# Kernel tuning notes

Measured on AMD Instinct MI355X. Metric: run time of the kernel, lower is better.

Reference implementation:

```python
import jax, jax.numpy as jnp
import numpy as np

SIZE = 512  # context size
T, D1, D2 = 32768, 512, 512
HID = int(SIZE * 1.5)  # 768, units of the 'context_linear' Dense


def setup_inputs() -> dict:
    key = jax.random.key(0)
    ks = jax.random.split(key, 8)
    din = D1 + D2
    return {
        "x1": jax.random.normal(ks[0], (T, D1), jnp.float32),
        "x2": jax.random.normal(ks[1], (T, D2), jnp.float32),
        "context0": jax.random.normal(ks[2], (1, SIZE), jnp.float32) * 0.1,  # tf.Variable init stddev=0.1
        "W_linear": jax.random.normal(ks[3], (din, HID), jnp.float32) * 0.02,
        "b_linear": jnp.zeros((HID,), jnp.float32),
        "W_embed": jax.random.normal(ks[4], (HID, SIZE), jnp.float32) * 0.02,
        "W_rate": jax.random.normal(ks[5], (SIZE, 1), jnp.float32) * 0.02,
        "W_forget": jax.random.normal(ks[6], (SIZE, SIZE), jnp.float32) * 0.02,
    }


def reference(x1, x2, context0, W_linear, b_linear, W_embed, W_rate, W_forget):
    # z = embed(linear(concat(inputs))) : Dense(1.5*size, linear) -> Dense(size, sigmoid, no bias)
    z = jnp.concatenate([x1, x2], axis=-1)                      # [T, D1+D2]
    z = jax.nn.sigmoid((z @ W_linear + b_linear) @ W_embed)     # [T, SIZE]
    # rate gate depends only on z_t, so precompute it in one GEMM
    r = jnp.tanh(z @ W_rate)[:, 0]                              # [T]

    # recurrence: c_t = softmax(c_{t-1} @ Wf) * c_{t-1} + r_t * z_t
    def step(c, zr):
        zt, rt = zr
        f = jax.nn.softmax(c @ W_forget)                        # [SIZE]
        c_new = f * c + rt * zt
        return c_new, c_new

    _, ys = jax.lax.scan(step, context0[0], (z, r))             # ys: [T, SIZE]
    return ys
```

## Files before the change

### kernel.cpp

```cpp
#include <hip/hip_runtime.h>
#include <stdint.h>
#include <stddef.h>


typedef __attribute__((ext_vector_type(8))) short bf16x8;
typedef __attribute__((ext_vector_type(4))) float f32x4;

__device__ __forceinline__ unsigned short f32_to_bf16(float f) {
  union { float f; unsigned u; } v; v.f = f;
  unsigned u = v.u;
  return (unsigned short)((u + 0x7fffu + ((u >> 16) & 1u)) >> 16);
}

__device__ __forceinline__ unsigned char f32_to_e4m3(float f) {
  float a = fabsf(f);
  unsigned char s = (unsigned char)((__float_as_uint(f) >> 24) & 0x80u);
  if (a >= 448.0f) return s | 0x7Eu;
  if (a < 0.015625f) {
    unsigned m = (unsigned)rintf(a * 512.0f);
    return s | (unsigned char)m;
  }
  unsigned u = __float_as_uint(a);
  unsigned r = u + 0x7FFFFu + ((u >> 20) & 1u);
  unsigned e = (r >> 23) - 120u;
  unsigned m = (r >> 20) & 7u;
  if (e >= 16u) return s | 0x7Eu;
  return s | (unsigned char)((e << 3) | m);
}

__device__ __forceinline__ void async16(const void* g, void* l) {
  __builtin_amdgcn_global_load_lds(
      (const __attribute__((address_space(1))) unsigned int*)g,
      (__attribute__((address_space(3))) unsigned int*)l, 16, 0, 0);
}

__global__ void k_convert_x(const float* __restrict__ x1, const float* __restrict__ x2,
                            unsigned short* __restrict__ Xb) {
  int id = blockIdx.x * 256 + threadIdx.x;
  int t  = id >> 8;
  int c4 = (id & 255) * 4;
  float4 v;
  if (c4 < 512) v = *(const float4*)(x1 + (size_t)t * 512 + c4);
  else          v = *(const float4*)(x2 + (size_t)t * 512 + (c4 - 512));
  ushort4 o;
  o.x = f32_to_bf16(v.x); o.y = f32_to_bf16(v.y);
  o.z = f32_to_bf16(v.z); o.w = f32_to_bf16(v.w);
  *(ushort4*)(Xb + (size_t)t * 1024 + c4) = o;
}

__global__ void k_transpose_w(const float* __restrict__ Wl, const float* __restrict__ We,
                              const float* __restrict__ Wf,
                              unsigned short* __restrict__ WlT,
                              unsigned short* __restrict__ WeT,
                              unsigned char* __restrict__ Wf8) {
  __shared__ float tile[32][33];
  int b = blockIdx.x;
  const float* src; int C, R, tr, tc, mode;
  if (b < 768)       { src = Wl; R = 1024; C = 768; tr = b / 24;  tc = b % 24;  mode = 0; }
  else if (b < 1152) { int j = b - 768;  src = We; R = 768; C = 512; tr = j / 16; tc = j % 16; mode = 1; }
  else               { int j = b - 1152; src = Wf; R = 512; C = 512; tr = j / 16; tc = j % 16; mode = 2; }
  const int tx = threadIdx.x & 31, ty = threadIdx.x >> 5;
  const int r0 = tr * 32, c0 = tc * 32;
#pragma unroll
  for (int p = 0; p < 4; ++p)
    tile[ty + p * 8][tx] = src[(size_t)(r0 + ty + p * 8) * C + c0 + tx];
  __syncthreads();
#pragma unroll
  for (int p = 0; p < 4; ++p) {
    int n = c0 + ty + p * 8;
    float v = tile[tx][ty + p * 8];
    if (mode == 0)      WlT[(size_t)n * 1024 + r0 + tx] = f32_to_bf16(v);
    else if (mode == 1) WeT[(size_t)n * 768  + r0 + tx] = f32_to_bf16(v);
    else                Wf8[(size_t)n * 512  + r0 + tx] = f32_to_e4m3(v * 16.0f);
  }
}

template <int MODE>
__global__ void k_gemm_bt(const unsigned short* __restrict__ A,
                          const unsigned short* __restrict__ Bt,
                          const float* __restrict__ bias,
                          unsigned short* __restrict__ Cb,
                          float* __restrict__ Cf,
                          int M, int N, int K) {
  __shared__ unsigned short As[128 * 32];
  __shared__ unsigned short Bs[128 * 32];
  const int tid = threadIdx.x;
  const int wv = tid >> 6, lane = tid & 63;
  const int nb = N >> 7;
  const int xcd = blockIdx.x & 7;
  const int s   = blockIdx.x >> 3;
  const int bm  = xcd * (M >> 10) + s / nb;
  const int bn  = s % nb;
  const int wm = wv >> 1, wn = wv & 1;
  f32x4 acc[4][4];
#pragma unroll
  for (int i = 0; i < 4; ++i)
#pragma unroll
    for (int j = 0; j < 4; ++j) acc[i][j] = f32x4{0.f, 0.f, 0.f, 0.f};

  const unsigned short* Ag = A + (size_t)(bm * 128 + (tid >> 2)) * K + (tid & 3) * 8;
  const unsigned short* Bg = Bt + (size_t)(bn * 128 + (tid >> 2)) * K + (tid & 3) * 8;
  unsigned short* AsW = As + wv * 512;
  unsigned short* BsW = Bs + wv * 512;
  const int lm = lane & 15;
  const int qk = (lane >> 4) * 8;

  for (int k0 = 0; k0 < K; k0 += 32) {
    __syncthreads();
    async16(Ag + k0,                  AsW);
    async16(Ag + k0 + (size_t)64 * K, AsW + 2048);
    async16(Bg + k0,                  BsW);
    async16(Bg + k0 + (size_t)64 * K, BsW + 2048);
    __syncthreads();
    bf16x8 af[4], bfr[4];
#pragma unroll
    for (int mt = 0; mt < 4; ++mt)
      af[mt] = *(const bf16x8*)(As + (wm * 64 + mt * 16 + lm) * 32 + qk);
#pragma unroll
    for (int nt = 0; nt < 4; ++nt)
      bfr[nt] = *(const bf16x8*)(Bs + (wn * 64 + nt * 16 + lm) * 32 + qk);
#pragma unroll
    for (int mt = 0; mt < 4; ++mt)
#pragma unroll
      for (int nt = 0; nt < 4; ++nt)
        acc[mt][nt] = __builtin_amdgcn_mfma_f32_16x16x32_bf16(af[mt], bfr[nt], acc[mt][nt], 0, 0, 0);
  }

  const int row0 = bm * 128 + wm * 64 + (lane >> 4) * 4;
  const int col0 = bn * 128 + wn * 64 + lm;
#pragma unroll
  for (int mt = 0; mt < 4; ++mt)
#pragma unroll
    for (int nt = 0; nt < 4; ++nt)
#pragma unroll
      for (int rr = 0; rr < 4; ++rr) {
        int row = row0 + mt * 16 + rr;
        int col = col0 + nt * 16;
        float v = acc[mt][nt][rr];
        if (MODE == 0) {
          v += bias[col];
          Cb[(size_t)row * N + col] = f32_to_bf16(v);
        } else {
          v = 1.0f / (1.0f + __expf(-v));
          Cf[(size_t)row * N + col] = v;
        }
      }
}

__global__ void k_rate(const float* __restrict__ Z, const float* __restrict__ Wr,
                       float* __restrict__ r) {
  const int lane = threadIdx.x & 63;
  const int t = blockIdx.x * 4 + (threadIdx.x >> 6);
  const float4* z4 = (const float4*)(Z + (size_t)t * 512 + lane * 8);
  const float4* w4 = (const float4*)(Wr + lane * 8);
  float4 za = z4[0], zb = z4[1], wa = w4[0], wb = w4[1];
  float acc = za.x * wa.x + za.y * wa.y + za.z * wa.z + za.w * wa.w +
              zb.x * wb.x + zb.y * wb.y + zb.z * wb.z + zb.w * wb.w;
#pragma unroll
  for (int off = 32; off > 0; off >>= 1) acc += __shfl_down(acc, off, 64);
  if (lane == 0) r[t] = tanhf(acc);
}

__global__ __launch_bounds__(1024) void k_recur(
    const unsigned char* __restrict__ Wf8, const float* __restrict__ Z,
    const float* __restrict__ rArr, const float* __restrict__ ctx0,
    float* __restrict__ out) {
  __shared__ unsigned char Cq[16 * 520];
  __shared__ float Lg[16 * 516];

  const int tid = threadIdx.x;
  const int wv = tid >> 6;
  const int lane = tid & 63;
  const int lm = lane & 15;
  const int qk = (lane >> 4) * 8;

  long Bf[2][16];
  const int nbase = wv * 32;
#pragma unroll
  for (int nt = 0; nt < 2; ++nt)
#pragma unroll
    for (int kt = 0; kt < 16; ++kt)
      Bf[nt][kt] = *(const long*)(Wf8 + (size_t)(nbase + nt * 16 + lm) * 512 + kt * 32 + qk);

  const int g = wv;
  const int cg = blockIdx.x * 16 + g;
  const int colBase = lane * 8;
  float c[8];
  if (cg == 0) {
#pragma unroll
    for (int j = 0; j < 8; ++j) c[j] = ctx0[colBase + j];
  } else {
#pragma unroll
    for (int j = 0; j < 8; ++j) c[j] = 0.f;
  }
  {
    unsigned long long pk = 0;
#pragma unroll
    for (int j = 0; j < 8; ++j)
      pk |= (unsigned long long)f32_to_e4m3(c[j] * 16.0f) << (8 * j);
    *(unsigned long long*)(Cq + g * 520 + colBase) = pk;
  }
  __syncthreads();

  for (int s = 0; s < 12; ++s) {
    f32x4 acc0 = {0.f, 0.f, 0.f, 0.f}, acc1 = {0.f, 0.f, 0.f, 0.f};
#pragma unroll
    for (int kt = 0; kt < 16; ++kt) {
      long a = *(const long*)(Cq + lm * 520 + kt * 32 + qk);
      acc0 = __builtin_amdgcn_mfma_f32_16x16x32_fp8_fp8(a, Bf[0][kt], acc0, 0, 0, 0);
      acc1 = __builtin_amdgcn_mfma_f32_16x16x32_fp8_fp8(a, Bf[1][kt], acc1, 0, 0, 0);
    }
#pragma unroll
    for (int rr = 0; rr < 4; ++rr) {
      Lg[((lane >> 4) * 4 + rr) * 516 + nbase + lm]      = acc0[rr];
      Lg[((lane >> 4) * 4 + rr) * 516 + nbase + 16 + lm] = acc1[rr];
    }
    __syncthreads();

    float l[8];
    const float* lg = Lg + g * 516 + colBase;
#pragma unroll
    for (int j = 0; j < 8; ++j) l[j] = lg[j] * (1.0f / 256.0f);
    float m = l[0];
#pragma unroll
    for (int j = 1; j < 8; ++j) m = fmaxf(m, l[j]);
#pragma unroll
    for (int off = 1; off < 64; off <<= 1) m = fmaxf(m, __shfl_xor(m, off, 64));
    float sum = 0.f;
#pragma unroll
    for (int j = 0; j < 8; ++j) { l[j] = __expf(l[j] - m); sum += l[j]; }
#pragma unroll
    for (int off = 1; off < 64; off <<= 1) sum += __shfl_xor(sum, off, 64);
    const float inv = 1.0f / sum;

    const int t = cg * 8 - 4 + s;
    if (t >= 0) {
      const float4* z4 = (const float4*)(Z + (size_t)t * 512 + colBase);
      float4 za = z4[0], zb = z4[1];
      float zz[8] = {za.x, za.y, za.z, za.w, zb.x, zb.y, zb.z, zb.w};
      const float rt = rArr[t];
#pragma unroll
      for (int j = 0; j < 8; ++j)
        c[j] = l[j] * inv * c[j] + rt * zz[j];
      if (s >= 4) {
        float4 o0 = {c[0], c[1], c[2], c[3]};
        float4 o1 = {c[4], c[5], c[6], c[7]};
        *(float4*)(out + (size_t)t * 512 + colBase)     = o0;
        *(float4*)(out + (size_t)t * 512 + colBase + 4) = o1;
      }
    }
    unsigned long long pk = 0;
#pragma unroll
    for (int j = 0; j < 8; ++j)
      pk |= (unsigned long long)f32_to_e4m3(c[j] * 16.0f) << (8 * j);
    *(unsigned long long*)(Cq + g * 520 + colBase) = pk;
    __syncthreads();
  }
}

extern "C" void kernel_launch(void* const* d_in, const int* in_sizes, int n_in,
                              void* d_out, int out_size, void* d_ws, size_t ws_size,
                              hipStream_t stream) {
  const float* x1   = (const float*)d_in[0];
  const float* x2   = (const float*)d_in[1];
  const float* ctx0 = (const float*)d_in[2];
  const float* Wl   = (const float*)d_in[3];
  const float* bl   = (const float*)d_in[4];
  const float* We   = (const float*)d_in[5];
  const float* Wr   = (const float*)d_in[6];
  const float* Wf   = (const float*)d_in[7];
  float* out = (float*)d_out;

  char* ws = (char*)d_ws;
  if (ws_size < 120193024u) return;
  unsigned short* Xb  = (unsigned short*)(ws);
  float*          Z32 = (float*)(ws);
  unsigned short* WlT = (unsigned short*)(ws + 67108864);
  unsigned short* WeT = (unsigned short*)(ws + 68681728);
  unsigned char*  Wf8 = (unsigned char*) (ws + 69468160);
  float*          rb  = (float*)         (ws + 69730304);
  unsigned short* H   = (unsigned short*)(ws + 69861376);

  k_convert_x<<<32768, 256, 0, stream>>>(x1, x2, Xb);
  k_transpose_w<<<1408, 256, 0, stream>>>(Wl, We, Wf, WlT, WeT, Wf8);
  k_gemm_bt<0><<<1536, 256, 0, stream>>>(Xb, WlT, bl, H, nullptr, 32768, 768, 1024);
  k_gemm_bt<1><<<1024, 256, 0, stream>>>(H, WeT, bl, nullptr, Z32, 32768, 512, 768);
  k_rate<<<8192, 256, 0, stream>>>(Z32, Wr, rb);
  k_recur<<<256, 1024, 0, stream>>>(Wf8, Z32, rb, ctx0, out);
}
```

Baseline: 356.7 us.

## Fuse rate projection into second GEMM epilogue and widen GEMM K-step to 64

```diff
diff --git a/kernel.cpp b/kernel.cpp
--- a/kernel.cpp
+++ b/kernel.cpp
@@ -52,13 +52,19 @@
                               const float* __restrict__ Wf,
                               unsigned short* __restrict__ WlT,
                               unsigned short* __restrict__ WeT,
-                              unsigned char* __restrict__ Wf8) {
+                              unsigned char* __restrict__ Wf8,
+                              float* __restrict__ rb) {
   __shared__ float tile[32][33];
   int b = blockIdx.x;
-  const float* src; int C, R, tr, tc, mode;
-  if (b < 768)       { src = Wl; R = 1024; C = 768; tr = b / 24;  tc = b % 24;  mode = 0; }
-  else if (b < 1152) { int j = b - 768;  src = We; R = 768; C = 512; tr = j / 16; tc = j % 16; mode = 1; }
-  else               { int j = b - 1152; src = Wf; R = 512; C = 512; tr = j / 16; tc = j % 16; mode = 2; }
+  if (b >= 1408) {
+    int idx = (b - 1408) * 256 + threadIdx.x;
+    *(float4*)(rb + idx * 4) = float4{0.f, 0.f, 0.f, 0.f};
+    return;
+  }
+  const float* src; int C, tr, tc, mode;
+  if (b < 768)       { src = Wl; C = 768; tr = b / 24;  tc = b % 24;  mode = 0; }
+  else if (b < 1152) { int j = b - 768;  src = We; C = 512; tr = j / 16; tc = j % 16; mode = 1; }
+  else               { int j = b - 1152; src = Wf; C = 512; tr = j / 16; tc = j % 16; mode = 2; }
   const int tx = threadIdx.x & 31, ty = threadIdx.x >> 5;
   const int r0 = tr * 32, c0 = tc * 32;
 #pragma unroll
@@ -78,12 +84,13 @@
 template <int MODE>
 __global__ void k_gemm_bt(const unsigned short* __restrict__ A,
                           const unsigned short* __restrict__ Bt,
-                          const float* __restrict__ bias,
+                          const float* __restrict__ aux,
                           unsigned short* __restrict__ Cb,
                           float* __restrict__ Cf,
+                          float* __restrict__ rate,
                           int M, int N, int K) {
-  __shared__ unsigned short As[128 * 32];
-  __shared__ unsigned short Bs[128 * 32];
+  __shared__ unsigned short As[128 * 64];
+  __shared__ unsigned short Bs[128 * 64];
   const int tid = threadIdx.x;
   const int wv = tid >> 6, lane = tid & 63;
   const int nb = N >> 7;
@@ -98,67 +105,79 @@
 #pragma unroll
     for (int j = 0; j < 4; ++j) acc[i][j] = f32x4{0.f, 0.f, 0.f, 0.f};
 
-  const unsigned short* Ag = A + (size_t)(bm * 128 + (tid >> 2)) * K + (tid & 3) * 8;
-  const unsigned short* Bg = Bt + (size_t)(bn * 128 + (tid >> 2)) * K + (tid & 3) * 8;
-  unsigned short* AsW = As + wv * 512;
-  unsigned short* BsW = Bs + wv * 512;
+  const unsigned short* Ag = A + (size_t)(bm * 128 + wv * 8 + (lane >> 3)) * K + (lane & 7) * 8;
+  const unsigned short* Bg = Bt + (size_t)(bn * 128 + wv * 8 + (lane >> 3)) * K + (lane & 7) * 8;
+  char* AsW = (char*)As + wv * 1024;
+  char* BsW = (char*)Bs + wv * 1024;
   const int lm = lane & 15;
   const int qk = (lane >> 4) * 8;
 
-  for (int k0 = 0; k0 < K; k0 += 32) {
+  for (int k0 = 0; k0 < K; k0 += 64) {
     __syncthreads();
-    async16(Ag + k0,                  AsW);
-    async16(Ag + k0 + (size_t)64 * K, AsW + 2048);
-    async16(Bg + k0,                  BsW);
-    async16(Bg + k0 + (size_t)64 * K, BsW + 2048);
+#pragma unroll
+    for (int p = 0; p < 4; ++p) {
+      async16(Ag + k0 + (size_t)(p * 32) * K, AsW + p * 4096);
+      async16(Bg + k0 + (size_t)(p * 32) * K, BsW + p * 4096);
+    }
     __syncthreads();
-    bf16x8 af[4], bfr[4];
-#pragma unroll
-    for (int mt = 0; mt < 4; ++mt)
-      af[mt] = *(const bf16x8*)(As + (wm * 64 + mt * 16 + lm) * 32 + qk);
-#pragma unroll
-    for (int nt = 0; nt < 4; ++nt)
-      bfr[nt] = *(const bf16x8*)(Bs + (wn * 64 + nt * 16 + lm) * 32 + qk);
-#pragma unroll
-    for (int mt = 0; mt < 4; ++mt)
+#pragma unroll
+    for (int ko = 0; ko < 2; ++ko) {
+      bf16x8 af[4], bfr[4];
+#pragma unroll
+      for (int mt = 0; mt < 4; ++mt)
+        af[mt] = *(const bf16x8*)(As + (wm * 64 + mt * 16 + lm) * 64 + ko * 32 + qk);
 #pragma unroll
       for (int nt = 0; nt < 4; ++nt)
-        acc[mt][nt] = __builtin_amdgcn_mfma_f32_16x16x32_bf16(af[mt], bfr[nt], acc[mt][nt], 0, 0, 0);
+        bfr[nt] = *(const bf16x8*)(Bs + (wn * 64 + nt * 16 + lm) * 64 + ko * 32 + qk);
+#pragma unroll
+      for (int mt = 0; mt < 4; ++mt)
+#pragma unroll
+        for (int nt = 0; nt < 4; ++nt)
+          acc[mt][nt] = __builtin_amdgcn_mfma_f32_16x16x32_bf16(af[mt], bfr[nt], acc[mt][nt], 0, 0, 0);
+    }
   }
 
   const int row0 = bm * 128 + wm * 64 + (lane >> 4) * 4;
   const int col0 = bn * 128 + wn * 64 + lm;
-#pragma unroll
-  for (int mt = 0; mt < 4; ++mt)
-#pragma unroll
-    for (int nt = 0; nt < 4; ++nt)
+  if (MODE == 0) {
+#pragma unroll
+    for (int mt = 0; mt < 4; ++mt)
+#pragma unroll
+      for (int nt = 0; nt < 4; ++nt)
+#pragma unroll
+        for (int rr = 0; rr < 4; ++rr) {
+          int row = row0 + mt * 16 + rr;
+          int col = col0 + nt * 16;
+          Cb[(size_t)row * N + col] = f32_to_bf16(acc[mt][nt][rr] + aux[col]);
+        }
+  } else {
+    float wr[4];
+#pragma unroll
+    for (int nt = 0; nt < 4; ++nt) wr[nt] = aux[col0 + nt * 16];
+#pragma unroll
+    for (int mt = 0; mt < 4; ++mt) {
+      float rsum[4] = {0.f, 0.f, 0.f, 0.f};
+#pragma unroll
+      for (int nt = 0; nt < 4; ++nt)
+#pragma unroll
+        for (int rr = 0; rr < 4; ++rr) {
+          int row = row0 + mt * 16 + rr;
+          int col = col0 + nt * 16;
+          float v = 1.0f / (1.0f + __expf(-acc[mt][nt][rr]));
+          Cf[(size_t)row * N + col] = v;
+          rsum[rr] += v * wr[nt];
+        }
 #pragma unroll
       for (int rr = 0; rr < 4; ++rr) {
-        int row = row0 + mt * 16 + rr;
-        int col = col0 + nt * 16;
-        float v = acc[mt][nt][rr];
-        if (MODE == 0) {
-          v += bias[col];
-          Cb[(size_t)row * N + col] = f32_to_bf16(v);
-        } else {
-          v = 1.0f / (1.0f + __expf(-v));
-          Cf[(size_t)row * N + col] = v;
-        }
+        float sv = rsum[rr];
+        sv += __shfl_xor(sv, 1, 64);
+        sv += __shfl_xor(sv, 2, 64);
+        sv += __shfl_xor(sv, 4, 64);
+        sv += __shfl_xor(sv, 8, 64);
+        if (lm == 0) atomicAdd(&rate[row0 + mt * 16 + rr], sv);
       }
-}
-
-__global__ void k_rate(const float* __restrict__ Z, const float* __restrict__ Wr,
-                       float* __restrict__ r) {
-  const int lane = threadIdx.x & 63;
-  const int t = blockIdx.x * 4 + (threadIdx.x >> 6);
-  const float4* z4 = (const float4*)(Z + (size_t)t * 512 + lane * 8);
-  const float4* w4 = (const float4*)(Wr + lane * 8);
-  float4 za = z4[0], zb = z4[1], wa = w4[0], wb = w4[1];
-  float acc = za.x * wa.x + za.y * wa.y + za.z * wa.z + za.w * wa.w +
-              zb.x * wb.x + zb.y * wb.y + zb.z * wb.z + zb.w * wb.w;
-#pragma unroll
-  for (int off = 32; off > 0; off >>= 1) acc += __shfl_down(acc, off, 64);
-  if (lane == 0) r[t] = tanhf(acc);
+    }
+  }
 }
 
 __global__ __launch_bounds__(1024) void k_recur(
@@ -203,6 +222,15 @@
   __syncthreads();
 
   for (int s = 0; s < 12; ++s) {
+    const int t = cg * 8 - 4 + s;
+    float4 za = {0.f, 0.f, 0.f, 0.f}, zb = {0.f, 0.f, 0.f, 0.f};
+    float rt = 0.f;
+    if (t >= 0) {
+      const float4* z4 = (const float4*)(Z + (size_t)t * 512 + colBase);
+      za = z4[0]; zb = z4[1];
+      rt = tanhf(rArr[t]);
+    }
+
     f32x4 acc0 = {0.f, 0.f, 0.f, 0.f}, acc1 = {0.f, 0.f, 0.f, 0.f};
 #pragma unroll
     for (int kt = 0; kt < 16; ++kt) {
@@ -233,12 +261,8 @@
     for (int off = 1; off < 64; off <<= 1) sum += __shfl_xor(sum, off, 64);
     const float inv = 1.0f / sum;
 
-    const int t = cg * 8 - 4 + s;
     if (t >= 0) {
-      const float4* z4 = (const float4*)(Z + (size_t)t * 512 + colBase);
-      float4 za = z4[0], zb = z4[1];
       float zz[8] = {za.x, za.y, za.z, za.w, zb.x, zb.y, zb.z, zb.w};
-      const float rt = rArr[t];
 #pragma unroll
       for (int j = 0; j < 8; ++j)
         c[j] = l[j] * inv * c[j] + rt * zz[j];
@@ -282,9 +306,8 @@
   unsigned short* H   = (unsigned short*)(ws + 69861376);
 
   k_convert_x<<<32768, 256, 0, stream>>>(x1, x2, Xb);
-  k_transpose_w<<<1408, 256, 0, stream>>>(Wl, We, Wf, WlT, WeT, Wf8);
-  k_gemm_bt<0><<<1536, 256, 0, stream>>>(Xb, WlT, bl, H, nullptr, 32768, 768, 1024);
-  k_gemm_bt<1><<<1024, 256, 0, stream>>>(H, WeT, bl, nullptr, Z32, 32768, 512, 768);
-  k_rate<<<8192, 256, 0, stream>>>(Z32, Wr, rb);
+  k_transpose_w<<<1440, 256, 0, stream>>>(Wl, We, Wf, WlT, WeT, Wf8, rb);
+  k_gemm_bt<0><<<1536, 256, 0, stream>>>(Xb, WlT, bl, H, nullptr, nullptr, 32768, 768, 1024);
+  k_gemm_bt<1><<<1024, 256, 0, stream>>>(H, WeT, Wr, nullptr, Z32, rb, 32768, 512, 768);
   k_recur<<<256, 1024, 0, stream>>>(Wf8, Z32, rb, ctx0, out);
 }
```

New measurement: 346.4 us. 1.03x faster.
